# Optimization experiments

Measured on AMD Instinct MI355X. Metric: run time of the kernel, lower is better.

## Reference

```python
import jax, jax.numpy as jnp
import numpy as np

B, S, E, H, LD, P, NC = 4, 256, 256, 8, 128, 256, 2
N = S * P  # total points (static)
EPS = 1e-5


def setup_inputs() -> dict:
    key = jax.random.key(0)
    ks = jax.random.split(key, 12)
    r = lambda i, shape, s: jax.random.normal(ks[i], shape, jnp.float32) * s
    return dict(
        gl_feats=jax.random.normal(ks[0], (S, B, E), jnp.float32),
        lo_feats=jax.random.normal(ks[1], (B, N, LD), jnp.float32),
        centroids=jax.random.normal(ks[2], (B, S, 2), jnp.float32),
        np_cluster=jnp.full((S,), P, jnp.int32),
        fc1_w=r(3, (16, 2), 0.5), fc1_b=jnp.zeros(16, jnp.float32),
        fc2_w=r(4, (E, 16), 0.1), fc2_b=jnp.zeros(E, jnp.float32),
        in_proj_w=r(5, (3 * E, E), 0.05), in_proj_b=jnp.zeros(3 * E, jnp.float32),
        out_proj_w=r(6, (E, E), 0.05), out_proj_b=jnp.zeros(E, jnp.float32),
        conv2_w=r(7, (E // 2, LD + E), 0.05), conv2_b=jnp.zeros(E // 2, jnp.float32),
        bn2_gamma=jnp.ones(E // 2, jnp.float32), bn2_beta=jnp.zeros(E // 2, jnp.float32),
        bn2_mean=jnp.zeros(E // 2, jnp.float32), bn2_var=jnp.ones(E // 2, jnp.float32),
        conv3_w=r(8, (64, E // 2), 0.05), conv3_b=jnp.zeros(64, jnp.float32),
        bn3_gamma=jnp.ones(64, jnp.float32), bn3_beta=jnp.zeros(64, jnp.float32),
        bn3_mean=jnp.zeros(64, jnp.float32), bn3_var=jnp.ones(64, jnp.float32),
        conv4_w=r(9, (NC, 64), 0.05), conv4_b=jnp.zeros(NC, jnp.float32),
    )


def _bn(z, g, b, m, v):
    # inference-mode BatchNorm1d over the channel (last) axis
    return (z - m) * jax.lax.rsqrt(v + EPS) * g + b


def reference(gl_feats, lo_feats, centroids, np_cluster,
              fc1_w, fc1_b, fc2_w, fc2_b,
              in_proj_w, in_proj_b, out_proj_w, out_proj_b,
              conv2_w, conv2_b, bn2_gamma, bn2_beta, bn2_mean, bn2_var,
              conv3_w, conv3_b, bn3_gamma, bn3_beta, bn3_mean, bn3_var,
              conv4_w, conv4_b):
    # positional encoding of centroids: Linear(2,16) -> leaky_relu -> Linear(16,E)
    h = centroids @ fc1_w.T + fc1_b                      # [B,S,16]
    h = jnp.where(h >= 0, h, 0.01 * h)                   # leaky_relu_, slope 0.01
    pos = h @ fc2_w.T + fc2_b                            # [B,S,E]
    x = gl_feats.transpose(1, 0, 2) + pos                # [B,S,E] (torch MHA is seq-first)

    # MultiheadAttention (self-attn, eval-mode dropout=identity)
    qkv = x @ in_proj_w.T + in_proj_b                    # [B,S,3E]
    q, k, v = jnp.split(qkv, 3, axis=-1)
    dh = E // H
    qh = q.reshape(B, S, H, dh)
    kh = k.reshape(B, S, H, dh)
    vh = v.reshape(B, S, H, dh)
    scores = jnp.einsum('bqhd,bkhd->bhqk', qh, kh) * (1.0 / np.sqrt(dh))
    attn = jax.nn.softmax(scores, axis=-1)               # [B,H,S,S]
    ctx = jnp.einsum('bhqk,bkhd->bqhd', attn, vh).reshape(B, S, E)
    attn_out = ctx @ out_proj_w.T + out_proj_b           # [B,S,E]

    # segment-broadcast: replace the python repeat/cat loop with a gather
    cluster_ids = jnp.repeat(jnp.arange(S), np_cluster, total_repeat_length=N)  # [N]
    global_feat = attn_out[:, cluster_ids, :]            # [B,N,E]

    pc = jnp.concatenate([lo_feats, global_feat], axis=2)  # [B,N,LD+E]
    # 1x1 Conv1d == pointwise Linear over channels
    h2 = jax.nn.relu(_bn(pc @ conv2_w.T + conv2_b, bn2_gamma, bn2_beta, bn2_mean, bn2_var))
    h3 = jax.nn.relu(_bn(h2 @ conv3_w.T + conv3_b, bn3_gamma, bn3_beta, bn3_mean, bn3_var))
    out = h3 @ conv4_w.T + conv4_b                       # [B,N,NC]
    return out.transpose(0, 2, 1)                        # [B,NC,N] to match torch layout
```

## Files before the change

### kernel.cpp

```cpp
#include <hip/hip_runtime.h>

#define B_   4
#define S_   256
#define E_   256
#define H_   8
#define LD_  128
#define N_   65536
#define NC_  2

typedef __attribute__((ext_vector_type(8))) short s8v;
typedef __attribute__((ext_vector_type(4))) float f32x4;

__device__ __forceinline__ short f2bf(float f) {
  union { float f; unsigned u; } v; v.f = f;
  unsigned r = (v.u + 0x7FFFu + ((v.u >> 16) & 1u)) >> 16;
  return (short)r;
}
__device__ __forceinline__ float bf2f(short s) {
  union { float f; unsigned u; } v; v.u = ((unsigned)(unsigned short)s) << 16;
  return v.f;
}
__device__ __forceinline__ s8v pack8(float4 a, float4 b) {
  s8v r;
  r[0] = f2bf(a.x); r[1] = f2bf(a.y); r[2] = f2bf(a.z); r[3] = f2bf(a.w);
  r[4] = f2bf(b.x); r[5] = f2bf(b.y); r[6] = f2bf(b.z); r[7] = f2bf(b.w);
  return r;
}

__global__ __launch_bounds__(256) void prep_k(
    const int* __restrict__ npc, int* __restrict__ ids,
    const float* __restrict__ ipw, const float* __restrict__ opw,
    const float* __restrict__ w2, const float* __restrict__ w3,
    const float* __restrict__ b2, const float* __restrict__ g2,
    const float* __restrict__ be2, const float* __restrict__ mu2,
    const float* __restrict__ va2,
    const float* __restrict__ b3, const float* __restrict__ g3,
    const float* __restrict__ be3, const float* __restrict__ mu3,
    const float* __restrict__ va3,
    short* __restrict__ iph, short* __restrict__ ipl,
    short* __restrict__ oph, short* __restrict__ opl,
    short* __restrict__ w2bf, short* __restrict__ w3bf,
    float* __restrict__ sc2, float* __restrict__ sh2,
    float* __restrict__ sc3, float* __restrict__ sh3,
    const float* __restrict__ gl, const float* __restrict__ cen,
    const float* __restrict__ fc1w, const float* __restrict__ fc1b,
    const float* __restrict__ fc2w, const float* __restrict__ fc2b,
    short* __restrict__ Xhi, short* __restrict__ Xlo) {
  __shared__ int red[256];
  __shared__ float hsh[16];
  int bid = blockIdx.x, t = threadIdx.x;
  if (bid < 768) {
    int i = bid * 256 + t;
    if (i < 196608) {
      float v = ipw[i]; short h = f2bf(v);
      iph[i] = h; ipl[i] = f2bf(v - bf2f(h));
    }
    if (i < 65536) {
      float v = opw[i]; short h = f2bf(v);
      oph[i] = h; opl[i] = f2bf(v - bf2f(h));
    }
    if (i < 49152) w2bf[i] = f2bf(w2[i]);
    if (i < 8192)  w3bf[i] = f2bf(w3[i]);
    if (i < 128) {
      float sc = g2[i] * rsqrtf(va2[i] + 1e-5f);
      sc2[i] = sc; sh2[i] = (b2[i] - mu2[i]) * sc + be2[i];
    }
    if (i < 64) {
      float sc = g3[i] * rsqrtf(va3[i] + 1e-5f);
      sc3[i] = sc; sh3[i] = (b3[i] - mu3[i]) * sc + be3[i];
    }
  } else if (bid <= 1024) {
    int s = bid - 768;
    int val = (s == 256) ? npc[t] : ((t < s) ? npc[t] : 0);
    red[t] = val;
    __syncthreads();
    for (int off = 128; off > 0; off >>= 1) {
      if (t < off) red[t] += red[t + off];
      __syncthreads();
    }
    int st = red[0];
    if (s < 256) {
      int en = st + npc[s]; if (en > N_) en = N_;
      for (int n = st + t; n < en; n += 256) ids[n] = s;
    } else {
      for (int n = st + t; n < N_; n += 256) ids[n] = 255;
    }
  } else {
    int bs = bid - 1025;
    int b = bs >> 8, s = bs & 255;
    if (t < 16) {
      float c0 = cen[bs * 2 + 0], c1 = cen[bs * 2 + 1];
      float v = c0 * fc1w[2 * t] + c1 * fc1w[2 * t + 1] + fc1b[t];
      hsh[t] = (v >= 0.f) ? v : 0.01f * v;
    }
    __syncthreads();
    float p = fc2b[t];
#pragma unroll
    for (int j = 0; j < 16; j++) p += hsh[j] * fc2w[t * 16 + j];
    float v = gl[((size_t)s * B_ + b) * E_ + t] + p;
    short h = f2bf(v);
    Xhi[(size_t)bs * E_ + t] = h;
    Xlo[(size_t)bs * E_ + t] = f2bf(v - bf2f(h));
  }
}

__global__ __launch_bounds__(256) void gemm_x3_k(
    const short* __restrict__ Ah, const short* __restrict__ Al,
    const short* __restrict__ Wh, const short* __restrict__ Wl,
    const float* __restrict__ bias, float* __restrict__ Cf,
    int M, int N, int K) {
  __shared__ __align__(16) short gs[18432];
  const int AH = 0, AL = 4608, WH = 9216, WL = 13824;
  int t = threadIdx.x;
  int row0 = blockIdx.x * 64, col0 = blockIdx.y * 64;
  int w = t >> 6, l = t & 63, quad = l >> 4, lr = l & 15;
  int m0 = w * 16;
  int ar = t >> 2, aq = (t & 3) * 16;
  f32x4 acc[4];
#pragma unroll
  for (int i = 0; i < 4; i++) acc[i] = (f32x4)(0.f);

  for (int kc = 0; kc < K; kc += 64) {
    __syncthreads();
    {
      size_t ra = (size_t)(row0 + ar) * K + kc + aq;
      size_t rw = (size_t)(col0 + ar) * K + kc + aq;
      *(s8v*)&gs[AH + ar * 72 + aq]     = *(const s8v*)&Ah[ra];
      *(s8v*)&gs[AH + ar * 72 + aq + 8] = *(const s8v*)&Ah[ra + 8];
      *(s8v*)&gs[AL + ar * 72 + aq]     = *(const s8v*)&Al[ra];
      *(s8v*)&gs[AL + ar * 72 + aq + 8] = *(const s8v*)&Al[ra + 8];
      *(s8v*)&gs[WH + ar * 72 + aq]     = *(const s8v*)&Wh[rw];
      *(s8v*)&gs[WH + ar * 72 + aq + 8] = *(const s8v*)&Wh[rw + 8];
      *(s8v*)&gs[WL + ar * 72 + aq]     = *(const s8v*)&Wl[rw];
      *(s8v*)&gs[WL + ar * 72 + aq + 8] = *(const s8v*)&Wl[rw + 8];
    }
    __syncthreads();
#pragma unroll
    for (int ks = 0; ks < 2; ks++) {
      int ko = ks * 32 + quad * 8;
      s8v ah = *(const s8v*)&gs[AH + (m0 + lr) * 72 + ko];
      s8v al = *(const s8v*)&gs[AL + (m0 + lr) * 72 + ko];
#pragma unroll
      for (int ct = 0; ct < 4; ct++) {
        s8v bh = *(const s8v*)&gs[WH + (ct * 16 + lr) * 72 + ko];
        s8v bl = *(const s8v*)&gs[WL + (ct * 16 + lr) * 72 + ko];
        acc[ct] = __builtin_amdgcn_mfma_f32_16x16x32_bf16(ah, bh, acc[ct], 0, 0, 0);
        acc[ct] = __builtin_amdgcn_mfma_f32_16x16x32_bf16(al, bh, acc[ct], 0, 0, 0);
        acc[ct] = __builtin_amdgcn_mfma_f32_16x16x32_bf16(ah, bl, acc[ct], 0, 0, 0);
      }
    }
  }
#pragma unroll
  for (int ct = 0; ct < 4; ct++) {
    int c = col0 + ct * 16 + lr;
    float bb = bias[c];
#pragma unroll
    for (int rg = 0; rg < 4; rg++) {
      int r = row0 + m0 + quad * 4 + rg;
      Cf[(size_t)r * N + c] = acc[ct][rg] + bb;
    }
  }
}

__global__ __launch_bounds__(256) void attn_k(const float* __restrict__ qkv,
                                              short* __restrict__ Chi,
                                              short* __restrict__ Clo) {
  int bid = blockIdx.x;
  int qt = bid & 7, h = (bid >> 3) & 7, b = bid >> 6;
  __shared__ __align__(16) float smem[16384];
  float* Kx = smem;
  float* Vx = smem + 8192;
  int t = threadIdx.x;
#pragma unroll
  for (int i = 0; i < 8; i++) {
    int row = i * 32 + (t >> 3);
    int d4 = (t & 7) * 4;
    const float* base = qkv + (size_t)(b * S_ + row) * 768 + h * 32 + d4;
    *(float4*)&Kx[row * 32 + d4] = *(const float4*)(base + 256);
    *(float4*)&Vx[row * 32 + d4] = *(const float4*)(base + 512);
  }
  int r = t & 31, g = t >> 5;
  float q[32];
  {
    const float* qb = qkv + (size_t)(b * S_ + qt * 32 + r) * 768 + h * 32;
#pragma unroll
    for (int d4 = 0; d4 < 32; d4 += 4) {
      float4 v = *(const float4*)(qb + d4);
      q[d4] = v.x; q[d4 + 1] = v.y; q[d4 + 2] = v.z; q[d4 + 3] = v.w;
    }
  }
  __syncthreads();
  const float scale = 0.17677669529663687f;
  int kk0 = g * 32;
  float sc[32];
  float m = -1e30f;
#pragma unroll
  for (int kk = 0; kk < 32; kk++) {
    const float* kr = &Kx[(kk0 + kk) * 32];
    float4 a = (float4){0.f, 0.f, 0.f, 0.f};
#pragma unroll
    for (int d4 = 0; d4 < 32; d4 += 4) {
      float4 kv = *(const float4*)(kr + d4);
      a.x += q[d4] * kv.x; a.y += q[d4 + 1] * kv.y;
      a.z += q[d4 + 2] * kv.z; a.w += q[d4 + 3] * kv.w;
    }
    float s = ((a.x + a.y) + (a.z + a.w)) * scale;
    sc[kk] = s;
    m = fmaxf(m, s);
  }
  float lsum = 0.f;
  float ctx[32];
#pragma unroll
  for (int d = 0; d < 32; d++) ctx[d] = 0.f;
#pragma unroll
  for (int kk = 0; kk < 32; kk++) {
    const float* vr = &Vx[(kk0 + kk) * 32];
    float p = __expf(sc[kk] - m);
    lsum += p;
#pragma unroll
    for (int d4 = 0; d4 < 32; d4 += 4) {
      float4 vv = *(const float4*)(vr + d4);
      ctx[d4] += p * vv.x; ctx[d4 + 1] += p * vv.y;
      ctx[d4 + 2] += p * vv.z; ctx[d4 + 3] += p * vv.w;
    }
  }
  __syncthreads();
  float* ctxbuf = smem;
  float* mbuf = smem + 8192;
  float* lbuf = smem + 8448;
  mbuf[g * 32 + r] = m;
  lbuf[g * 32 + r] = lsum;
#pragma unroll
  for (int d = 0; d < 32; d++)
    ctxbuf[(g * 32 + r) * 32 + ((d + r) & 31)] = ctx[d];
  __syncthreads();
  int r2 = t & 31, dq = t >> 5;
  float M = -1e30f;
#pragma unroll
  for (int gg = 0; gg < 8; gg++) M = fmaxf(M, mbuf[gg * 32 + r2]);
  float wg[8]; float L = 0.f;
#pragma unroll
  for (int gg = 0; gg < 8; gg++) {
    wg[gg] = __expf(mbuf[gg * 32 + r2] - M);
    L += lbuf[gg * 32 + r2] * wg[gg];
  }
  float invL = 1.f / L;
  size_t base = (size_t)(b * S_ + qt * 32 + r2) * E_ + h * 32;
#pragma unroll
  for (int dd = 0; dd < 4; dd++) {
    int d = dq * 4 + dd;
    float o = 0.f;
#pragma unroll
    for (int gg = 0; gg < 8; gg++)
      o += ctxbuf[(gg * 32 + r2) * 32 + ((d + r2) & 31)] * wg[gg];
    o *= invL;
    short hi = f2bf(o);
    Chi[base + d] = hi;
    Clo[base + d] = f2bf(o - bf2f(hi));
  }
}

__global__ __launch_bounds__(256) void opg_k(
    const short* __restrict__ Chi, const short* __restrict__ Clo,
    const short* __restrict__ oph, const short* __restrict__ opl,
    const float* __restrict__ opb, const short* __restrict__ w2bf,
    float* __restrict__ G) {
  __shared__ __align__(16) short gsm[50688];
  const int AH = 0, AL = 4608, WH = 9216, WL = 27648;
  const int CT = 0, W2B = 16896;
  int t = threadIdx.x;
  int row0 = blockIdx.x * 64;
  int w = t >> 6, l = t & 63, quad = l >> 4, lr = l & 15;

  f32x4 acc[16];
#pragma unroll
  for (int i = 0; i < 16; i++) acc[i] = (f32x4)(0.f);

  for (int kc = 0; kc < 256; kc += 64) {
    __syncthreads();
    {
#pragma unroll
      for (int j = 0; j < 8; j++) {
        *(s8v*)&gsm[WH + t * 72 + j * 8] = *(const s8v*)&oph[(size_t)t * 256 + kc + j * 8];
        *(s8v*)&gsm[WL + t * 72 + j * 8] = *(const s8v*)&opl[(size_t)t * 256 + kc + j * 8];
      }
      if (t < 128) {
        int row = t >> 1, half = (t & 1) * 32;
        size_t ra = (size_t)(row0 + row) * 256 + kc + half;
#pragma unroll
        for (int j = 0; j < 4; j++) {
          *(s8v*)&gsm[AH + row * 72 + half + j * 8] = *(const s8v*)&Chi[ra + j * 8];
          *(s8v*)&gsm[AL + row * 72 + half + j * 8] = *(const s8v*)&Clo[ra + j * 8];
        }
      }
    }
    __syncthreads();
#pragma unroll
    for (int ks = 0; ks < 2; ks++) {
      int ko = ks * 32 + quad * 8;
      s8v ah = *(const s8v*)&gsm[AH + (w * 16 + lr) * 72 + ko];
      s8v al = *(const s8v*)&gsm[AL + (w * 16 + lr) * 72 + ko];
#pragma unroll
      for (int ct = 0; ct < 16; ct++) {
        s8v bh = *(const s8v*)&gsm[WH + (ct * 16 + lr) * 72 + ko];
        s8v bl = *(const s8v*)&gsm[WL + (ct * 16 + lr) * 72 + ko];
        acc[ct] = __builtin_amdgcn_mfma_f32_16x16x32_bf16(ah, bh, acc[ct], 0, 0, 0);
        acc[ct] = __builtin_amdgcn_mfma_f32_16x16x32_bf16(al, bh, acc[ct], 0, 0, 0);
        acc[ct] = __builtin_amdgcn_mfma_f32_16x16x32_bf16(ah, bl, acc[ct], 0, 0, 0);
      }
    }
  }
  __syncthreads();
#pragma unroll
  for (int ct = 0; ct < 16; ct++) {
    int c = ct * 16 + lr;
    float bb = opb[c];
#pragma unroll
    for (int rg = 0; rg < 4; rg++) {
      int r = w * 16 + quad * 4 + rg;
      gsm[CT + r * 264 + c] = f2bf(acc[ct][rg] + bb);
    }
  }
  {
    int ch = t >> 1, koff = (t & 1) * 128;
#pragma unroll
    for (int j = 0; j < 16; j++)
      *(s8v*)&gsm[W2B + ch * 264 + koff + j * 8] =
          *(const s8v*)&w2bf[(size_t)ch * 384 + 128 + koff + j * 8];
  }
  __syncthreads();
  f32x4 acc2[8];
#pragma unroll
  for (int i = 0; i < 8; i++) acc2[i] = (f32x4)(0.f);
#pragma unroll
  for (int ks = 0; ks < 8; ks++) {
    int ko = ks * 32 + quad * 8;
    s8v a = *(const s8v*)&gsm[CT + (w * 16 + lr) * 264 + ko];
#pragma unroll
    for (int ct = 0; ct < 8; ct++) {
      s8v b = *(const s8v*)&gsm[W2B + (ct * 16 + lr) * 264 + ko];
      acc2[ct] = __builtin_amdgcn_mfma_f32_16x16x32_bf16(a, b, acc2[ct], 0, 0, 0);
    }
  }
#pragma unroll
  for (int ct = 0; ct < 8; ct++) {
    int c = ct * 16 + lr;
#pragma unroll
    for (int rg = 0; rg < 4; rg++) {
      int r = row0 + w * 16 + quad * 4 + rg;
      G[(size_t)r * 128 + c] = acc2[ct][rg];
    }
  }
}

#define CF_SW2 0
#define CF_SA  17408
#define CF_H2  0
#define CF_SW3 17408
#define CF_H3  0

__global__ __launch_bounds__(256, 3) void conv_fused_k(
    const float* __restrict__ lo, const float* __restrict__ G,
    const int* __restrict__ ids,
    const short* __restrict__ w2bf, const short* __restrict__ w3bf,
    const float* __restrict__ sc2, const float* __restrict__ sh2,
    const float* __restrict__ sc3, const float* __restrict__ sh3,
    const float* __restrict__ w4, const float* __restrict__ b4,
    float* __restrict__ out) {
  __shared__ __align__(16) short smem[26624];
  __shared__ int lds_ids[128];
  int t = threadIdx.x;
  int bid = blockIdx.x;
  int b = bid >> 9;
  int n0 = (bid & 511) << 7;
  int w = t >> 6, l = t & 63;
  int quad = l >> 4, lr = l & 15;
  int mh = w & 1, chh = w >> 1;
  int ar = t >> 1, akh = (t & 1) * 32;
  const float* lob = &lo[((size_t)b * N_ + n0 + ar) * LD_ + akh];

  {
    int ch = t >> 1, koff = (t & 1) * 64;
#pragma unroll
    for (int j = 0; j < 8; j++)
      *(s8v*)&smem[CF_SW2 + ch * 136 + koff + j * 8] =
          *(const s8v*)&w2bf[(size_t)ch * 384 + koff + j * 8];
  }
  if (t < 128) lds_ids[t] = ids[n0 + t];
  float4 pf[8];
#pragma unroll
  for (int j = 0; j < 8; j++) pf[j] = *(const float4*)(lob + j * 4);
#pragma unroll
  for (int j = 0; j < 4; j++)
    *(s8v*)&smem[CF_SA + ar * 72 + akh + j * 8] = pack8(pf[2 * j], pf[2 * j + 1]);
  __syncthreads();

#pragma unroll
  for (int j = 0; j < 8; j++) pf[j] = *(const float4*)(lob + 64 + j * 4);

  f32x4 acc2[4][4];
#pragma unroll
  for (int i = 0; i < 4; i++)
#pragma unroll
    for (int j = 0; j < 4; j++) acc2[i][j] = (f32x4)(0.f);

#pragma unroll
  for (int ks = 0; ks < 2; ks++) {
    int ko = ks * 32 + quad * 8;
    s8v af[4], bf[4];
#pragma unroll
    for (int mt = 0; mt < 4; mt++)
      af[mt] = *(const s8v*)&smem[CF_SA + (64 * mh + 16 * mt + lr) * 72 + ko];
#pragma unroll
    for (int ct = 0; ct < 4; ct++)
      bf[ct] = *(const s8v*)&smem[CF_SW2 + (64 * chh + 16 * ct + lr) * 136 + ko];
#pragma unroll
    for (int mt = 0; mt < 4; mt++)
#pragma unroll
      for (int ct = 0; ct < 4; ct++)
        acc2[mt][ct] = __builtin_amdgcn_mfma_f32_16x16x32_bf16(af[mt], bf[ct], acc2[mt][ct], 0, 0, 0);
  }
  __syncthreads();
#pragma unroll
  for (int j = 0; j < 4; j++)
    *(s8v*)&smem[CF_SA + ar * 72 + akh + j * 8] = pack8(pf[2 * j], pf[2 * j + 1]);
  __syncthreads();
#pragma unroll
  for (int ks = 0; ks < 2; ks++) {
    int koA = ks * 32 + quad * 8;
    int koW = 64 + koA;
    s8v af[4], bf[4];
#pragma unroll
    for (int mt = 0; mt < 4; mt++)
      af[mt] = *(const s8v*)&smem[CF_SA + (64 * mh + 16 * mt + lr) * 72 + koA];
#pragma unroll
    for (int ct = 0; ct < 4; ct++)
      bf[ct] = *(const s8v*)&smem[CF_SW2 + (64 * chh + 16 * ct + lr) * 136 + koW];
#pragma unroll
    for (int mt = 0; mt < 4; mt++)
#pragma unroll
      for (int ct = 0; ct < 4; ct++)
        acc2[mt][ct] = __builtin_amdgcn_mfma_f32_16x16x32_bf16(af[mt], bf[ct], acc2[mt][ct], 0, 0, 0);
  }
  __syncthreads();

#pragma unroll
  for (int ct = 0; ct < 4; ct++) {
    int c = 64 * chh + 16 * ct + lr;
    float sc = sc2[c], sh = sh2[c];
    float gv[4][4];
#pragma unroll
    for (int mt = 0; mt < 4; mt++)
#pragma unroll
      for (int rg = 0; rg < 4; rg++) {
        int p = 64 * mh + 16 * mt + 4 * quad + rg;
        gv[mt][rg] = G[((size_t)b * 256 + lds_ids[p]) * 128 + c];
      }
#pragma unroll
    for (int mt = 0; mt < 4; mt++)
#pragma unroll
      for (int rg = 0; rg < 4; rg++) {
        int p = 64 * mh + 16 * mt + 4 * quad + rg;
        float z = (acc2[mt][ct][rg] + gv[mt][rg]) * sc + sh;
        smem[CF_H2 + p * 136 + c] = f2bf(fmaxf(z, 0.f));
      }
  }
  {
    int ch = t >> 2, kq = (t & 3) * 32;
#pragma unroll
    for (int j = 0; j < 4; j++)
      *(s8v*)&smem[CF_SW3 + ch * 136 + kq + j * 8] =
          *(const s8v*)&w3bf[ch * 128 + kq + j * 8];
  }
  __syncthreads();

  f32x4 acc3[2][4];
#pragma unroll
  for (int i = 0; i < 2; i++)
#pragma unroll
    for (int j = 0; j < 4; j++) acc3[i][j] = (f32x4)(0.f);
#pragma unroll
  for (int ks = 0; ks < 4; ks++) {
    int ko = ks * 32 + quad * 8;
    s8v af[2], bf[4];
#pragma unroll
    for (int mt = 0; mt < 2; mt++)
      af[mt] = *(const s8v*)&smem[CF_H2 + (32 * w + 16 * mt + lr) * 136 + ko];
#pragma unroll
    for (int ct = 0; ct < 4; ct++)
      bf[ct] = *(const s8v*)&smem[CF_SW3 + (16 * ct + lr) * 136 + ko];
#pragma unroll
    for (int mt = 0; mt < 2; mt++)
#pragma unroll
      for (int ct = 0; ct < 4; ct++)
        acc3[mt][ct] = __builtin_amdgcn_mfma_f32_16x16x32_bf16(af[mt], bf[ct], acc3[mt][ct], 0, 0, 0);
  }
  __syncthreads();

#pragma unroll
  for (int ct = 0; ct < 4; ct++) {
    int c = 16 * ct + lr;
    float sc = sc3[c], sh = sh3[c];
#pragma unroll
    for (int mt = 0; mt < 2; mt++)
#pragma unroll
      for (int rg = 0; rg < 4; rg++) {
        int p = 32 * w + 16 * mt + 4 * quad + rg;
        float z = acc3[mt][ct][rg] * sc + sh;
        smem[CF_H3 + p * 72 + c] = f2bf(fmaxf(z, 0.f));
      }
  }
  __syncthreads();

  {
    int c = t >> 7, p = t & 127;
    float s = b4[c];
#pragma unroll
    for (int j = 0; j < 8; j++) {
      s8v hv = *(const s8v*)&smem[CF_H3 + p * 72 + j * 8];
#pragma unroll
      for (int e = 0; e < 8; e++)
        s += bf2f(hv[e]) * w4[c * 64 + j * 8 + e];
    }
    out[((size_t)b * NC_ + c) * N_ + n0 + p] = s;
  }
}

extern "C" void kernel_launch(void* const* d_in, const int* in_sizes, int n_in,
                              void* d_out, int out_size, void* d_ws, size_t ws_size,
                              hipStream_t stream) {
  const float* gl   = (const float*)d_in[0];
  const float* lo   = (const float*)d_in[1];
  const float* cen  = (const float*)d_in[2];
  const int*   npc  = (const int*)d_in[3];
  const float* fc1w = (const float*)d_in[4];
  const float* fc1b = (const float*)d_in[5];
  const float* fc2w = (const float*)d_in[6];
  const float* fc2b = (const float*)d_in[7];
  const float* ipw  = (const float*)d_in[8];
  const float* ipb  = (const float*)d_in[9];
  const float* opw  = (const float*)d_in[10];
  const float* opb  = (const float*)d_in[11];
  const float* w2   = (const float*)d_in[12];
  const float* b2   = (const float*)d_in[13];
  const float* g2   = (const float*)d_in[14];
  const float* be2  = (const float*)d_in[15];
  const float* mu2  = (const float*)d_in[16];
  const float* va2  = (const float*)d_in[17];
  const float* w3   = (const float*)d_in[18];
  const float* b3   = (const float*)d_in[19];
  const float* g3   = (const float*)d_in[20];
  const float* be3  = (const float*)d_in[21];
  const float* mu3  = (const float*)d_in[22];
  const float* va3  = (const float*)d_in[23];
  const float* w4   = (const float*)d_in[24];
  const float* b4   = (const float*)d_in[25];

  char* ws = (char*)d_ws;
  float* qkv  = (float*)(ws);
  short* Xhi  = (short*)(ws + 3145728);
  short* Xlo  = (short*)(ws + 3670016);
  short* Chi  = (short*)(ws + 4194304);
  short* Clo  = (short*)(ws + 4718592);
  float* G    = (float*)(ws + 5242880);
  short* iph  = (short*)(ws + 5767168);
  short* ipl  = (short*)(ws + 6160384);
  short* oph  = (short*)(ws + 6553600);
  short* opl  = (short*)(ws + 6684672);
  short* w2bf = (short*)(ws + 6815744);
  short* w3bf = (short*)(ws + 6914048);
  int*   ids  = (int*)  (ws + 6930432);
  float* sc2  = (float*)(ws + 7192576);
  float* sh2  = (float*)(ws + 7193088);
  float* sc3  = (float*)(ws + 7193600);
  float* sh3  = (float*)(ws + 7193856);
  float* out  = (float*)d_out;

  prep_k<<<2049, 256, 0, stream>>>(npc, ids, ipw, opw, w2, w3,
                                   b2, g2, be2, mu2, va2,
                                   b3, g3, be3, mu3, va3,
                                   iph, ipl, oph, opl, w2bf, w3bf,
                                   sc2, sh2, sc3, sh3,
                                   gl, cen, fc1w, fc1b, fc2w, fc2b, Xhi, Xlo);
  gemm_x3_k<<<dim3(16, 12), 256, 0, stream>>>(Xhi, Xlo, iph, ipl, ipb,
                                              qkv, B_ * S_, 768, E_);
  attn_k<<<B_ * H_ * 8, 256, 0, stream>>>(qkv, Chi, Clo);
  opg_k<<<16, 256, 0, stream>>>(Chi, Clo, oph, opl, opb, w2bf, G);
  conv_fused_k<<<B_ * (N_ / 128), 256, 0, stream>>>(
      lo, G, ids, w2bf, w3bf, sc2, sh2, sc3, sh3, w4, b4, out);
}
```

Measured before the change: 307.0 us.

## Split out-proj/G GEMM into two tiled kernels and slim conv_fused LDS usage

The single 16-block opg_k kernel is replaced by two kernels: a 64x64-tiled out-projection GEMM (64 blocks) that writes bf16 output into reused workspace, and a separate GEMM producing G (32 blocks). This spreads the small GEMMs over more CUs. In conv_fused_k, w2 and w3 fragments are now read directly from global/L2 instead of being staged in LDS. The gathered G values preload the accumulator, and all 128 lo channels are packed in one pass. LDS drops enough to allow 4 blocks per CU, and pack8 uses the packed v_cvt_pk_bf16_f32 instruction. The cost is one extra launch and uncached global fragment loads inside the MFMA loop.

Measured after the change: 301.2 us. About the same (-1.9%).

```diff
diff --git a/kernel.cpp b/kernel.cpp
--- a/kernel.cpp
+++ b/kernel.cpp
@@ -21,10 +21,12 @@
   return v.f;
 }
 __device__ __forceinline__ s8v pack8(float4 a, float4 b) {
-  s8v r;
-  r[0] = f2bf(a.x); r[1] = f2bf(a.y); r[2] = f2bf(a.z); r[3] = f2bf(a.w);
-  r[4] = f2bf(b.x); r[5] = f2bf(b.y); r[6] = f2bf(b.z); r[7] = f2bf(b.w);
-  return r;
+  union { s8v s; unsigned u[4]; } r;
+  asm("v_cvt_pk_bf16_f32 %0, %1, %2" : "=v"(r.u[0]) : "v"(a.x), "v"(a.y));
+  asm("v_cvt_pk_bf16_f32 %0, %1, %2" : "=v"(r.u[1]) : "v"(a.z), "v"(a.w));
+  asm("v_cvt_pk_bf16_f32 %0, %1, %2" : "=v"(r.u[2]) : "v"(b.x), "v"(b.y));
+  asm("v_cvt_pk_bf16_f32 %0, %1, %2" : "=v"(r.u[3]) : "v"(b.z), "v"(b.w));
+  return r.s;
 }
 
 __global__ __launch_bounds__(256) void prep_k(
@@ -162,6 +164,111 @@
   }
 }
 
+__global__ __launch_bounds__(256) void opgemm_k(
+    const short* __restrict__ Ah, const short* __restrict__ Al,
+    const short* __restrict__ Wh, const short* __restrict__ Wl,
+    const float* __restrict__ bias, short* __restrict__ Cb,
+    int M, int N, int K) {
+  __shared__ __align__(16) short gs[18432];
+  const int AH = 0, AL = 4608, WH = 9216, WL = 13824;
+  int t = threadIdx.x;
+  int row0 = blockIdx.x * 64, col0 = blockIdx.y * 64;
+  int w = t >> 6, l = t & 63, quad = l >> 4, lr = l & 15;
+  int m0 = w * 16;
+  int ar = t >> 2, aq = (t & 3) * 16;
+  f32x4 acc[4];
+#pragma unroll
+  for (int i = 0; i < 4; i++) acc[i] = (f32x4)(0.f);
+
+  for (int kc = 0; kc < K; kc += 64) {
+    __syncthreads();
+    {
+      size_t ra = (size_t)(row0 + ar) * K + kc + aq;
+      size_t rw = (size_t)(col0 + ar) * K + kc + aq;
+      *(s8v*)&gs[AH + ar * 72 + aq]     = *(const s8v*)&Ah[ra];
+      *(s8v*)&gs[AH + ar * 72 + aq + 8] = *(const s8v*)&Ah[ra + 8];
+      *(s8v*)&gs[AL + ar * 72 + aq]     = *(const s8v*)&Al[ra];
+      *(s8v*)&gs[AL + ar * 72 + aq + 8] = *(const s8v*)&Al[ra + 8];
+      *(s8v*)&gs[WH + ar * 72 + aq]     = *(const s8v*)&Wh[rw];
+      *(s8v*)&gs[WH + ar * 72 + aq + 8] = *(const s8v*)&Wh[rw + 8];
+      *(s8v*)&gs[WL + ar * 72 + aq]     = *(const s8v*)&Wl[rw];
+      *(s8v*)&gs[WL + ar * 72 + aq + 8] = *(const s8v*)&Wl[rw + 8];
+    }
+    __syncthreads();
+#pragma unroll
+    for (int ks = 0; ks < 2; ks++) {
+      int ko = ks * 32 + quad * 8;
+      s8v ah = *(const s8v*)&gs[AH + (m0 + lr) * 72 + ko];
+      s8v al = *(const s8v*)&gs[AL + (m0 + lr) * 72 + ko];
+#pragma unroll
+      for (int ct = 0; ct < 4; ct++) {
+        s8v bh = *(const s8v*)&gs[WH + (ct * 16 + lr) * 72 + ko];
+        s8v bl = *(const s8v*)&gs[WL + (ct * 16 + lr) * 72 + ko];
+        acc[ct] = __builtin_amdgcn_mfma_f32_16x16x32_bf16(ah, bh, acc[ct], 0, 0, 0);
+        acc[ct] = __builtin_amdgcn_mfma_f32_16x16x32_bf16(al, bh, acc[ct], 0, 0, 0);
+        acc[ct] = __builtin_amdgcn_mfma_f32_16x16x32_bf16(ah, bl, acc[ct], 0, 0, 0);
+      }
+    }
+  }
+#pragma unroll
+  for (int ct = 0; ct < 4; ct++) {
+    int c = col0 + ct * 16 + lr;
+    float bb = bias[c];
+#pragma unroll
+    for (int rg = 0; rg < 4; rg++) {
+      int r = row0 + m0 + quad * 4 + rg;
+      Cb[(size_t)r * N + c] = f2bf(acc[ct][rg] + bb);
+    }
+  }
+}
+
+__global__ __launch_bounds__(256) void gbf_k(
+    const short* __restrict__ A, const short* __restrict__ w2bf,
+    float* __restrict__ C) {
+  __shared__ __align__(16) short gs[9216];
+  const int AH = 0, BH = 4608;
+  int t = threadIdx.x;
+  int row0 = blockIdx.x * 64, col0 = blockIdx.y * 64;
+  int w = t >> 6, l = t & 63, quad = l >> 4, lr = l & 15;
+  int m0 = w * 16;
+  int ar = t >> 2, aq = (t & 3) * 16;
+  f32x4 acc[4];
+#pragma unroll
+  for (int i = 0; i < 4; i++) acc[i] = (f32x4)(0.f);
+
+  for (int kc = 0; kc < 256; kc += 64) {
+    __syncthreads();
+    {
+      size_t ra = (size_t)(row0 + ar) * 256 + kc + aq;
+      size_t rb = (size_t)(col0 + ar) * 384 + 128 + kc + aq;
+      *(s8v*)&gs[AH + ar * 72 + aq]     = *(const s8v*)&A[ra];
+      *(s8v*)&gs[AH + ar * 72 + aq + 8] = *(const s8v*)&A[ra + 8];
+      *(s8v*)&gs[BH + ar * 72 + aq]     = *(const s8v*)&w2bf[rb];
+      *(s8v*)&gs[BH + ar * 72 + aq + 8] = *(const s8v*)&w2bf[rb + 8];
+    }
+    __syncthreads();
+#pragma unroll
+    for (int ks = 0; ks < 2; ks++) {
+      int ko = ks * 32 + quad * 8;
+      s8v a = *(const s8v*)&gs[AH + (m0 + lr) * 72 + ko];
+#pragma unroll
+      for (int ct = 0; ct < 4; ct++) {
+        s8v b = *(const s8v*)&gs[BH + (ct * 16 + lr) * 72 + ko];
+        acc[ct] = __builtin_amdgcn_mfma_f32_16x16x32_bf16(a, b, acc[ct], 0, 0, 0);
+      }
+    }
+  }
+#pragma unroll
+  for (int ct = 0; ct < 4; ct++) {
+    int c = col0 + ct * 16 + lr;
+#pragma unroll
+    for (int rg = 0; rg < 4; rg++) {
+      int r = row0 + m0 + quad * 4 + rg;
+      C[(size_t)r * 128 + c] = acc[ct][rg];
+    }
+  }
+}
+
 __global__ __launch_bounds__(256) void attn_k(const float* __restrict__ qkv,
                                               short* __restrict__ Chi,
                                               short* __restrict__ Clo) {
@@ -260,106 +367,7 @@
   }
 }
 
-__global__ __launch_bounds__(256) void opg_k(
-    const short* __restrict__ Chi, const short* __restrict__ Clo,
-    const short* __restrict__ oph, const short* __restrict__ opl,
-    const float* __restrict__ opb, const short* __restrict__ w2bf,
-    float* __restrict__ G) {
-  __shared__ __align__(16) short gsm[50688];
-  const int AH = 0, AL = 4608, WH = 9216, WL = 27648;
-  const int CT = 0, W2B = 16896;
-  int t = threadIdx.x;
-  int row0 = blockIdx.x * 64;
-  int w = t >> 6, l = t & 63, quad = l >> 4, lr = l & 15;
-
-  f32x4 acc[16];
-#pragma unroll
-  for (int i = 0; i < 16; i++) acc[i] = (f32x4)(0.f);
-
-  for (int kc = 0; kc < 256; kc += 64) {
-    __syncthreads();
-    {
-#pragma unroll
-      for (int j = 0; j < 8; j++) {
-        *(s8v*)&gsm[WH + t * 72 + j * 8] = *(const s8v*)&oph[(size_t)t * 256 + kc + j * 8];
-        *(s8v*)&gsm[WL + t * 72 + j * 8] = *(const s8v*)&opl[(size_t)t * 256 + kc + j * 8];
-      }
-      if (t < 128) {
-        int row = t >> 1, half = (t & 1) * 32;
-        size_t ra = (size_t)(row0 + row) * 256 + kc + half;
-#pragma unroll
-        for (int j = 0; j < 4; j++) {
-          *(s8v*)&gsm[AH + row * 72 + half + j * 8] = *(const s8v*)&Chi[ra + j * 8];
-          *(s8v*)&gsm[AL + row * 72 + half + j * 8] = *(const s8v*)&Clo[ra + j * 8];
-        }
-      }
-    }
-    __syncthreads();
-#pragma unroll
-    for (int ks = 0; ks < 2; ks++) {
-      int ko = ks * 32 + quad * 8;
-      s8v ah = *(const s8v*)&gsm[AH + (w * 16 + lr) * 72 + ko];
-      s8v al = *(const s8v*)&gsm[AL + (w * 16 + lr) * 72 + ko];
-#pragma unroll
-      for (int ct = 0; ct < 16; ct++) {
-        s8v bh = *(const s8v*)&gsm[WH + (ct * 16 + lr) * 72 + ko];
-        s8v bl = *(const s8v*)&gsm[WL + (ct * 16 + lr) * 72 + ko];
-        acc[ct] = __builtin_amdgcn_mfma_f32_16x16x32_bf16(ah, bh, acc[ct], 0, 0, 0);
-        acc[ct] = __builtin_amdgcn_mfma_f32_16x16x32_bf16(al, bh, acc[ct], 0, 0, 0);
-        acc[ct] = __builtin_amdgcn_mfma_f32_16x16x32_bf16(ah, bl, acc[ct], 0, 0, 0);
-      }
-    }
-  }
-  __syncthreads();
-#pragma unroll
-  for (int ct = 0; ct < 16; ct++) {
-    int c = ct * 16 + lr;
-    float bb = opb[c];
-#pragma unroll
-    for (int rg = 0; rg < 4; rg++) {
-      int r = w * 16 + quad * 4 + rg;
-      gsm[CT + r * 264 + c] = f2bf(acc[ct][rg] + bb);
-    }
-  }
-  {
-    int ch = t >> 1, koff = (t & 1) * 128;
-#pragma unroll
-    for (int j = 0; j < 16; j++)
-      *(s8v*)&gsm[W2B + ch * 264 + koff + j * 8] =
-          *(const s8v*)&w2bf[(size_t)ch * 384 + 128 + koff + j * 8];
-  }
-  __syncthreads();
-  f32x4 acc2[8];
-#pragma unroll
-  for (int i = 0; i < 8; i++) acc2[i] = (f32x4)(0.f);
-#pragma unroll
-  for (int ks = 0; ks < 8; ks++) {
-    int ko = ks * 32 + quad * 8;
-    s8v a = *(const s8v*)&gsm[CT + (w * 16 + lr) * 264 + ko];
-#pragma unroll
-    for (int ct = 0; ct < 8; ct++) {
-      s8v b = *(const s8v*)&gsm[W2B + (ct * 16 + lr) * 264 + ko];
-      acc2[ct] = __builtin_amdgcn_mfma_f32_16x16x32_bf16(a, b, acc2[ct], 0, 0, 0);
-    }
-  }
-#pragma unroll
-  for (int ct = 0; ct < 8; ct++) {
-    int c = ct * 16 + lr;
-#pragma unroll
-    for (int rg = 0; rg < 4; rg++) {
-      int r = row0 + w * 16 + quad * 4 + rg;
-      G[(size_t)r * 128 + c] = acc2[ct][rg];
-    }
-  }
-}
-
-#define CF_SW2 0
-#define CF_SA  17408
-#define CF_H2  0
-#define CF_SW3 17408
-#define CF_H3  0
-
-__global__ __launch_bounds__(256, 3) void conv_fused_k(
+__global__ __launch_bounds__(256, 4) void conv_fused_k(
     const float* __restrict__ lo, const float* __restrict__ G,
     const int* __restrict__ ids,
     const short* __restrict__ w2bf, const short* __restrict__ w3bf,
@@ -367,7 +375,7 @@
     const float* __restrict__ sc3, const float* __restrict__ sh3,
     const float* __restrict__ w4, const float* __restrict__ b4,
     float* __restrict__ out) {
-  __shared__ __align__(16) short smem[26624];
+  __shared__ __align__(16) short smem[17408];
   __shared__ int lds_ids[128];
   int t = threadIdx.x;
   int bid = blockIdx.x;
@@ -376,71 +384,52 @@
   int w = t >> 6, l = t & 63;
   int quad = l >> 4, lr = l & 15;
   int mh = w & 1, chh = w >> 1;
-  int ar = t >> 1, akh = (t & 1) * 32;
+  int ar = t >> 1, akh = (t & 1) * 64;
   const float* lob = &lo[((size_t)b * N_ + n0 + ar) * LD_ + akh];
 
+  if (t < 128) lds_ids[t] = ids[n0 + t];
   {
-    int ch = t >> 1, koff = (t & 1) * 64;
-#pragma unroll
-    for (int j = 0; j < 8; j++)
-      *(s8v*)&smem[CF_SW2 + ch * 136 + koff + j * 8] =
-          *(const s8v*)&w2bf[(size_t)ch * 384 + koff + j * 8];
-  }
-  if (t < 128) lds_ids[t] = ids[n0 + t];
-  float4 pf[8];
-#pragma unroll
-  for (int j = 0; j < 8; j++) pf[j] = *(const float4*)(lob + j * 4);
-#pragma unroll
-  for (int j = 0; j < 4; j++)
-    *(s8v*)&smem[CF_SA + ar * 72 + akh + j * 8] = pack8(pf[2 * j], pf[2 * j + 1]);
-  __syncthreads();
-
-#pragma unroll
-  for (int j = 0; j < 8; j++) pf[j] = *(const float4*)(lob + 64 + j * 4);
+    float4 pf[8];
+#pragma unroll
+    for (int j = 0; j < 8; j++) pf[j] = *(const float4*)(lob + j * 4);
+#pragma unroll
+    for (int j = 0; j < 4; j++)
+      *(s8v*)&smem[ar * 136 + akh + j * 8] = pack8(pf[2 * j], pf[2 * j + 1]);
+#pragma unroll
+    for (int j = 0; j < 8; j++) pf[j] = *(const float4*)(lob + 32 + j * 4);
+#pragma unroll
+    for (int j = 0; j < 4; j++)
+      *(s8v*)&smem[ar * 136 + akh + 32 + j * 8] = pack8(pf[2 * j], pf[2 * j + 1]);
+  }
+  __syncthreads();
 
   f32x4 acc2[4][4];
 #pragma unroll
-  for (int i = 0; i < 4; i++)
-#pragma unroll
-    for (int j = 0; j < 4; j++) acc2[i][j] = (f32x4)(0.f);
-
-#pragma unroll
-  for (int ks = 0; ks < 2; ks++) {
+  for (int mt = 0; mt < 4; mt++)
+#pragma unroll
+    for (int rg = 0; rg < 4; rg++) {
+      int p = 64 * mh + 16 * mt + 4 * quad + rg;
+      const float* gr = &G[((size_t)b * 256 + lds_ids[p]) * 128 + 64 * chh + lr];
+#pragma unroll
+      for (int ct = 0; ct < 4; ct++)
+        acc2[mt][ct][rg] = gr[16 * ct];
+    }
+
+#pragma unroll
+  for (int ks = 0; ks < 4; ks++) {
     int ko = ks * 32 + quad * 8;
-    s8v af[4], bf[4];
+    s8v af[4], bfr[4];
 #pragma unroll
     for (int mt = 0; mt < 4; mt++)
-      af[mt] = *(const s8v*)&smem[CF_SA + (64 * mh + 16 * mt + lr) * 72 + ko];
+      af[mt] = *(const s8v*)&smem[(64 * mh + 16 * mt + lr) * 136 + ko];
 #pragma unroll
     for (int ct = 0; ct < 4; ct++)
-      bf[ct] = *(const s8v*)&smem[CF_SW2 + (64 * chh + 16 * ct + lr) * 136 + ko];
+      bfr[ct] = *(const s8v*)&w2bf[(size_t)(64 * chh + 16 * ct + lr) * 384 + ko];
 #pragma unroll
     for (int mt = 0; mt < 4; mt++)
 #pragma unroll
       for (int ct = 0; ct < 4; ct++)
-        acc2[mt][ct] = __builtin_amdgcn_mfma_f32_16x16x32_bf16(af[mt], bf[ct], acc2[mt][ct], 0, 0, 0);
-  }
-  __syncthreads();
-#pragma unroll
-  for (int j = 0; j < 4; j++)
-    *(s8v*)&smem[CF_SA + ar * 72 + akh + j * 8] = pack8(pf[2 * j], pf[2 * j + 1]);
-  __syncthreads();
-#pragma unroll
-  for (int ks = 0; ks < 2; ks++) {
-    int koA = ks * 32 + quad * 8;
-    int koW = 64 + koA;
-    s8v af[4], bf[4];
-#pragma unroll
-    for (int mt = 0; mt < 4; mt++)
-      af[mt] = *(const s8v*)&smem[CF_SA + (64 * mh + 16 * mt + lr) * 72 + koA];
-#pragma unroll
-    for (int ct = 0; ct < 4; ct++)
-      bf[ct] = *(const s8v*)&smem[CF_SW2 + (64 * chh + 16 * ct + lr) * 136 + koW];
-#pragma unroll
-    for (int mt = 0; mt < 4; mt++)
-#pragma unroll
-      for (int ct = 0; ct < 4; ct++)
-        acc2[mt][ct] = __builtin_amdgcn_mfma_f32_16x16x32_bf16(af[mt], bf[ct], acc2[mt][ct], 0, 0, 0);
+        acc2[mt][ct] = __builtin_amdgcn_mfma_f32_16x16x32_bf16(af[mt], bfr[ct], acc2[mt][ct], 0, 0, 0);
   }
   __syncthreads();
 
@@ -448,29 +437,14 @@
   for (int ct = 0; ct < 4; ct++) {
     int c = 64 * chh + 16 * ct + lr;
     float sc = sc2[c], sh = sh2[c];
-    float gv[4][4];
 #pragma unroll
     for (int mt = 0; mt < 4; mt++)
 #pragma unroll
       for (int rg = 0; rg < 4; rg++) {
         int p = 64 * mh + 16 * mt + 4 * quad + rg;
-        gv[mt][rg] = G[((size_t)b * 256 + lds_ids[p]) * 128 + c];
+        float z = acc2[mt][ct][rg] * sc + sh;
+        smem[p * 136 + c] = f2bf(fmaxf(z, 0.f));
       }
-#pragma unroll
-    for (int mt = 0; mt < 4; mt++)
-#pragma unroll
-      for (int rg = 0; rg < 4; rg++) {
-        int p = 64 * mh + 16 * mt + 4 * quad + rg;
-        float z = (acc2[mt][ct][rg] + gv[mt][rg]) * sc + sh;
-        smem[CF_H2 + p * 136 + c] = f2bf(fmaxf(z, 0.f));
-      }
-  }
-  {
-    int ch = t >> 2, kq = (t & 3) * 32;
-#pragma unroll
-    for (int j = 0; j < 4; j++)
-      *(s8v*)&smem[CF_SW3 + ch * 136 + kq + j * 8] =
-          *(const s8v*)&w3bf[ch * 128 + kq + j * 8];
   }
   __syncthreads();
 
@@ -482,18 +456,18 @@
 #pragma unroll
   for (int ks = 0; ks < 4; ks++) {
     int ko = ks * 32 + quad * 8;
-    s8v af[2], bf[4];
+    s8v af2[2], bf3[4];
 #pragma unroll
     for (int mt = 0; mt < 2; mt++)
-      af[mt] = *(const s8v*)&smem[CF_H2 + (32 * w + 16 * mt + lr) * 136 + ko];
+      af2[mt] = *(const s8v*)&smem[(32 * w + 16 * mt + lr) * 136 + ko];
 #pragma unroll
     for (int ct = 0; ct < 4; ct++)
-      bf[ct] = *(const s8v*)&smem[CF_SW3 + (16 * ct + lr) * 136 + ko];
+      bf3[ct] = *(const s8v*)&w3bf[(size_t)(16 * ct + lr) * 128 + ko];
 #pragma unroll
     for (int mt = 0; mt < 2; mt++)
 #pragma unroll
       for (int ct = 0; ct < 4; ct++)
-        acc3[mt][ct] = __builtin_amdgcn_mfma_f32_16x16x32_bf16(af[mt], bf[ct], acc3[mt][ct], 0, 0, 0);
+        acc3[mt][ct] = __builtin_amdgcn_mfma_f32_16x16x32_bf16(af2[mt], bf3[ct], acc3[mt][ct], 0, 0, 0);
   }
   __syncthreads();
 
@@ -507,7 +481,7 @@
       for (int rg = 0; rg < 4; rg++) {
         int p = 32 * w + 16 * mt + 4 * quad + rg;
         float z = acc3[mt][ct][rg] * sc + sh;
-        smem[CF_H3 + p * 72 + c] = f2bf(fmaxf(z, 0.f));
+        smem[p * 72 + c] = f2bf(fmaxf(z, 0.f));
       }
   }
   __syncthreads();
@@ -517,7 +491,7 @@
     float s = b4[c];
 #pragma unroll
     for (int j = 0; j < 8; j++) {
-      s8v hv = *(const s8v*)&smem[CF_H3 + p * 72 + j * 8];
+      s8v hv = *(const s8v*)&smem[p * 72 + j * 8];
 #pragma unroll
       for (int e = 0; e < 8; e++)
         s += bf2f(hv[e]) * w4[c * 64 + j * 8 + e];
@@ -558,6 +532,7 @@
 
   char* ws = (char*)d_ws;
   float* qkv  = (float*)(ws);
+  short* AO   = (short*)(ws);
   short* Xhi  = (short*)(ws + 3145728);
   short* Xlo  = (short*)(ws + 3670016);
   short* Chi  = (short*)(ws + 4194304);
@@ -585,7 +560,9 @@
   gemm_x3_k<<<dim3(16, 12), 256, 0, stream>>>(Xhi, Xlo, iph, ipl, ipb,
                                               qkv, B_ * S_, 768, E_);
   attn_k<<<B_ * H_ * 8, 256, 0, stream>>>(qkv, Chi, Clo);
-  opg_k<<<16, 256, 0, stream>>>(Chi, Clo, oph, opl, opb, w2bf, G);
+  opgemm_k<<<dim3(16, 4), 256, 0, stream>>>(Chi, Clo, oph, opl, opb, AO,
+                                            B_ * S_, 256, E_);
+  gbf_k<<<dim3(16, 2), 256, 0, stream>>>(AO, w2bf, G);
   conv_fused_k<<<B_ * (N_ / 128), 256, 0, stream>>>(
       lo, G, ids, w2bf, w3bf, sc2, sh2, sc3, sh3, w4, b4, out);
 }
```
